# Optimization experiments

Measured on AMD Instinct MI355X. Metric: run time of the kernel, lower is better.

The kernel has to match this reference:

```python
import jax, jax.numpy as jnp
import numpy as np

N_NODES = 100000
N_EDGES = 3200000


def gcn_conv(x, row, col, W, n):
    # PyG GCNConv: x @ W, then D^{-1/2}(A+I)D^{-1/2} aggregation (self-loops added).
    h = x @ W  # [N, out]
    loop = jnp.arange(n)
    r = jnp.concatenate([row, loop])
    c = jnp.concatenate([col, loop])
    deg = jax.ops.segment_sum(jnp.ones_like(c, dtype=h.dtype), c, num_segments=n)
    dinv = jnp.where(deg > 0, jax.lax.rsqrt(deg), 0.0)
    norm = dinv[r] * dinv[c]  # [E+N]
    msg = h[r] * norm[:, None]  # gather + scale
    return jax.ops.segment_sum(msg, c, num_segments=n)  # scatter-add


def setup_inputs() -> dict:
    key = jax.random.key(0)
    k1, k2, k3, k4, k5 = jax.random.split(key, 5)
    x = jax.random.normal(k1, (N_NODES, 1), dtype=jnp.float32)
    edge_index = jax.random.randint(k2, (2, N_EDGES), 0, N_NODES, dtype=jnp.int64)
    W1 = jax.random.normal(k3, (1, 16), dtype=jnp.float32) * 0.5
    W2 = jax.random.normal(k4, (16, 16), dtype=jnp.float32) * 0.25
    W3 = jax.random.normal(k5, (16, 11), dtype=jnp.float32) * 0.25
    b = jnp.zeros((11,), dtype=jnp.float32)
    return {"x": x, "edge_index": edge_index, "W1": W1, "W2": W2, "W3": W3, "b": b}


def reference(x, edge_index, W1, W2, W3, b):
    n = x.shape[0]
    row, col = edge_index[0], edge_index[1]
    h = jax.nn.relu(gcn_conv(x, row, col, W1, n))
    h = jax.nn.relu(gcn_conv(h, row, col, W2, n))
    g = jnp.mean(h, axis=0).reshape(-1, 16)  # [1,16] graph readout
    out = (g @ W3).squeeze() + b  # [11]
    return out
```

## Files before the change

### kernel.cpp

```cpp
#include <hip/hip_runtime.h>

static constexpr int N = 100000;
static constexpr int E = 3200000;
static constexpr int BUKSHIFT = 8;
static constexpr int BUKSZ = 1 << BUKSHIFT;
static constexpr int BUKMASK = BUKSZ - 1;
static constexpr int NBUK = (N + BUKSZ - 1) / BUKSZ;
static constexpr int CAP = 12288;
static constexpr int GSTRIDE = 16;
static constexpr int SC_CHUNK = 4096;
static constexpr int SC_T = 512;
static constexpr int SC_BLOCKS = (E + SC_CHUNK - 1) / SC_CHUNK;


__global__ void k_init(int* __restrict__ gofs) {
    int i = blockIdx.x * blockDim.x + threadIdx.x;
    if (i < NBUK) gofs[i * GSTRIDE] = i * CAP;
}

__global__ __launch_bounds__(SC_T) void k_scatter(const int4* __restrict__ rows4,
                                                  const int4* __restrict__ cols4,
                                                  int* __restrict__ gofs,
                                                  int* __restrict__ binned) {
    __shared__ int hist[4 * NBUK];
    __shared__ int gbase[NBUK];

    const int tid = threadIdx.x;
    const int g = tid >> 7;
    for (int i = tid; i < 4 * NBUK; i += SC_T) hist[i] = 0;
    __syncthreads();

    const int nI4 = E / 4;
    const int base4 = blockIdx.x * (SC_CHUNK / 4);
    const int ia = base4 + tid, ib = base4 + SC_T + tid;
    const bool va = ia < nI4, vb = ib < nI4;
    int4 ra, ca, rb, cb;
    if (va) { ra = rows4[ia]; ca = cols4[ia]; }
    if (vb) { rb = rows4[ib]; cb = cols4[ib]; }

    if (va) {
        atomicAdd(&hist[g * NBUK + (ca.x >> BUKSHIFT)], 1);
        atomicAdd(&hist[g * NBUK + (ca.y >> BUKSHIFT)], 1);
        atomicAdd(&hist[g * NBUK + (ca.z >> BUKSHIFT)], 1);
        atomicAdd(&hist[g * NBUK + (ca.w >> BUKSHIFT)], 1);
    }
    if (vb) {
        atomicAdd(&hist[g * NBUK + (cb.x >> BUKSHIFT)], 1);
        atomicAdd(&hist[g * NBUK + (cb.y >> BUKSHIFT)], 1);
        atomicAdd(&hist[g * NBUK + (cb.z >> BUKSHIFT)], 1);
        atomicAdd(&hist[g * NBUK + (cb.w >> BUKSHIFT)], 1);
    }
    __syncthreads();

    if (tid < NBUK) {
        int h0 = hist[0 * NBUK + tid], h1 = hist[1 * NBUK + tid];
        int h2 = hist[2 * NBUK + tid], h3 = hist[3 * NBUK + tid];
        hist[0 * NBUK + tid] = 0;
        hist[1 * NBUK + tid] = h0;
        hist[2 * NBUK + tid] = h0 + h1;
        hist[3 * NBUK + tid] = h0 + h1 + h2;
        int c = h0 + h1 + h2 + h3;
        gbase[tid] = c ? atomicAdd(&gofs[tid * GSTRIDE], c) : 0;
    }
    __syncthreads();

    if (va) {
        int b, off;
        b = ca.x >> BUKSHIFT; off = atomicAdd(&hist[g * NBUK + b], 1); binned[gbase[b] + off] = (ra.x << BUKSHIFT) | (ca.x & BUKMASK);
        b = ca.y >> BUKSHIFT; off = atomicAdd(&hist[g * NBUK + b], 1); binned[gbase[b] + off] = (ra.y << BUKSHIFT) | (ca.y & BUKMASK);
        b = ca.z >> BUKSHIFT; off = atomicAdd(&hist[g * NBUK + b], 1); binned[gbase[b] + off] = (ra.z << BUKSHIFT) | (ca.z & BUKMASK);
        b = ca.w >> BUKSHIFT; off = atomicAdd(&hist[g * NBUK + b], 1); binned[gbase[b] + off] = (ra.w << BUKSHIFT) | (ca.w & BUKMASK);
    }
    if (vb) {
        int b, off;
        b = cb.x >> BUKSHIFT; off = atomicAdd(&hist[g * NBUK + b], 1); binned[gbase[b] + off] = (rb.x << BUKSHIFT) | (cb.x & BUKMASK);
        b = cb.y >> BUKSHIFT; off = atomicAdd(&hist[g * NBUK + b], 1); binned[gbase[b] + off] = (rb.y << BUKSHIFT) | (cb.y & BUKMASK);
        b = cb.z >> BUKSHIFT; off = atomicAdd(&hist[g * NBUK + b], 1); binned[gbase[b] + off] = (rb.z << BUKSHIFT) | (cb.z & BUKMASK);
        b = cb.w >> BUKSHIFT; off = atomicAdd(&hist[g * NBUK + b], 1); binned[gbase[b] + off] = (rb.w << BUKSHIFT) | (cb.w & BUKMASK);
    }
}

__global__ __launch_bounds__(1024) void k_deg(const int* __restrict__ binned,
                                              const int* __restrict__ gofs,
                                              const float* __restrict__ x,
                                              float* __restrict__ dinv,
                                              float* __restrict__ y1) {
    __shared__ int cnt[8][BUKSZ];
    const int tid = threadIdx.x;
    for (int i = tid; i < 8 * BUKSZ; i += 1024) (&cnt[0][0])[i] = 0;
    __syncthreads();
    const int b = blockIdx.x, g = tid >> 7;
    const int s0 = b * CAP;
    const int n = gofs[b * GSTRIDE] - s0;
    const int n4 = n >> 2;
    const int4* b4 = (const int4*)(binned + s0);
    for (int i = tid; i < n4; i += 1024) {
        int4 p = b4[i];
        atomicAdd(&cnt[g][p.x & BUKMASK], 1);
        atomicAdd(&cnt[g][p.y & BUKMASK], 1);
        atomicAdd(&cnt[g][p.z & BUKMASK], 1);
        atomicAdd(&cnt[g][p.w & BUKMASK], 1);
    }
    if (tid < (n & 3)) atomicAdd(&cnt[g][binned[s0 + (n4 << 2) + tid] & BUKMASK], 1);
    __syncthreads();
    if (tid < BUKSZ) {
        int v = (b << BUKSHIFT) + tid;
        if (v < N) {
            int c = 0;
            #pragma unroll
            for (int q = 0; q < 8; ++q) c += cnt[q][tid];
            float d = rsqrtf(1.0f + (float)c);
            dinv[v] = d;
            y1[v] = d * x[v];
        }
    }
}

__global__ __launch_bounds__(1024) void k_acc1(const int* __restrict__ binned,
                                               const int* __restrict__ gofs,
                                               const float* __restrict__ y1,
                                               const float* __restrict__ dinv,
                                               float* __restrict__ m) {
    __shared__ float acc[8][BUKSZ];
    const int tid = threadIdx.x;
    for (int i = tid; i < 8 * BUKSZ; i += 1024) (&acc[0][0])[i] = 0.f;
    __syncthreads();
    const int b = blockIdx.x, g = tid >> 7;
    const int s0 = b * CAP;
    const int n = gofs[b * GSTRIDE] - s0;
    const int n4 = n >> 2;
    const int4* b4 = (const int4*)(binned + s0);
    for (int i = tid; i < n4; i += 1024) {
        int4 p = b4[i];
        atomicAdd(&acc[g][p.x & BUKMASK], y1[p.x >> BUKSHIFT]);
        atomicAdd(&acc[g][p.y & BUKMASK], y1[p.y >> BUKSHIFT]);
        atomicAdd(&acc[g][p.z & BUKMASK], y1[p.z >> BUKSHIFT]);
        atomicAdd(&acc[g][p.w & BUKMASK], y1[p.w >> BUKSHIFT]);
    }
    if (tid < (n & 3)) {
        int p = binned[s0 + (n4 << 2) + tid];
        atomicAdd(&acc[g][p & BUKMASK], y1[p >> BUKSHIFT]);
    }
    __syncthreads();
    if (tid < BUKSZ) {
        int v = (b << BUKSHIFT) + tid;
        if (v < N) {
            float a = 0.f;
            #pragma unroll
            for (int q = 0; q < 8; ++q) a += acc[q][tid];
            float d = dinv[v];
            float s = d * a + d * y1[v];
            m[v] = d * s;
        }
    }
}

__global__ __launch_bounds__(1024) void k_acc2(const int* __restrict__ binned,
                                               const int* __restrict__ gofs,
                                               const float* __restrict__ m,
                                               const float* __restrict__ dinv,
                                               const float* __restrict__ W1,
                                               const float* __restrict__ W2,
                                               float* __restrict__ partials) {
    __shared__ float tp[8][BUKSZ], tn[8][BUKSZ];
    __shared__ float sP[16], sM[16], sAcc[16];
    const int tid = threadIdx.x;
    if (tid < 16) {
        float p = 0.f, q = 0.f;
        for (int k = 0; k < 16; ++k) {
            float w1 = W1[k];
            float w2 = W2[k * 16 + tid];
            p += fmaxf(w1, 0.f) * w2;
            q += fminf(w1, 0.f) * w2;
        }
        sP[tid] = p; sM[tid] = q; sAcc[tid] = 0.f;
    }
    for (int i = tid; i < 8 * BUKSZ; i += 1024) { (&tp[0][0])[i] = 0.f; (&tn[0][0])[i] = 0.f; }
    __syncthreads();
    const int b = blockIdx.x, g = tid >> 7;
    const int s0 = b * CAP;
    const int n = gofs[b * GSTRIDE] - s0;
    const int n4 = n >> 2;
    const int4* b4 = (const int4*)(binned + s0);
    for (int i = tid; i < n4; i += 1024) {
        int4 p = b4[i];
        float v0 = m[p.x >> BUKSHIFT], v1 = m[p.y >> BUKSHIFT];
        float v2 = m[p.z >> BUKSHIFT], v3 = m[p.w >> BUKSHIFT];
        atomicAdd(v0 >= 0.f ? &tp[g][p.x & BUKMASK] : &tn[g][p.x & BUKMASK], v0);
        atomicAdd(v1 >= 0.f ? &tp[g][p.y & BUKMASK] : &tn[g][p.y & BUKMASK], v1);
        atomicAdd(v2 >= 0.f ? &tp[g][p.z & BUKMASK] : &tn[g][p.z & BUKMASK], v2);
        atomicAdd(v3 >= 0.f ? &tp[g][p.w & BUKMASK] : &tn[g][p.w & BUKMASK], v3);
    }
    if (tid < (n & 3)) {
        int p = binned[s0 + (n4 << 2) + tid];
        float val = m[p >> BUKSHIFT];
        atomicAdd(val >= 0.f ? &tp[g][p & BUKMASK] : &tn[g][p & BUKMASK], val);
    }
    __syncthreads();
    float alpha = 0.f, beta = 0.f;
    if (tid < BUKSZ) {
        int v = (b << BUKSHIFT) + tid;
        if (v < N) {
            float a = 0.f, bb = 0.f;
            #pragma unroll
            for (int q = 0; q < 8; ++q) { a += tp[q][tid]; bb += tn[q][tid]; }
            float d = dinv[v], mv = m[v];
            alpha = d * a;
            beta  = d * bb;
            float self = d * mv;
            if (mv >= 0.f) alpha += self; else beta += self;
        }
    }
    const int lane = tid & 63;
    for (int j = 0; j < 16; ++j) {
        float h = fmaxf(alpha * sP[j] + beta * sM[j], 0.f);
        #pragma unroll
        for (int off = 32; off > 0; off >>= 1) h += __shfl_down(h, off);
        if (lane == 0 && h != 0.f) atomicAdd(&sAcc[j], h);
    }
    __syncthreads();
    if (tid < 16) partials[b * 16 + tid] = sAcc[tid];
}

__global__ void k_out(const float* __restrict__ partials, const float* __restrict__ W3,
                      const float* __restrict__ b, float* __restrict__ out) {
    __shared__ float s[16][16];
    int j = threadIdx.x & 15;
    int g = threadIdx.x >> 4;
    float acc = 0.f;
    for (int blk = g; blk < NBUK; blk += 16) acc += partials[blk * 16 + j];
    s[g][j] = acc;
    __syncthreads();
    if (threadIdx.x < 16) {
        float tot = 0.f;
        #pragma unroll
        for (int gg = 0; gg < 16; ++gg) tot += s[gg][threadIdx.x];
        s[0][threadIdx.x] = tot * (1.0f / (float)N);
    }
    __syncthreads();
    if (threadIdx.x < 11) {
        float acc2 = b[threadIdx.x];
        #pragma unroll
        for (int k = 0; k < 16; ++k) acc2 += s[0][k] * W3[k * 11 + threadIdx.x];
        out[threadIdx.x] = acc2;
    }
}

extern "C" void kernel_launch(void* const* d_in, const int* in_sizes, int n_in,
                              void* d_out, int out_size, void* d_ws, size_t ws_size,
                              hipStream_t stream) {
    const float* x  = (const float*)d_in[0];
    const int*   ei = (const int*)d_in[1];
    const float* W1 = (const float*)d_in[2];
    const float* W2 = (const float*)d_in[3];
    const float* W3 = (const float*)d_in[4];
    const float* b  = (const float*)d_in[5];
    float* out = (float*)d_out;

    int*   wsi      = (int*)d_ws;
    int*   binned   = wsi;
    float* dinv     = (float*)(wsi + (size_t)NBUK * CAP);
    float* y1       = dinv + N;
    float* m        = y1 + N;
    int*   gofs     = (int*)(m + N);
    float* partials = (float*)(gofs + NBUK * GSTRIDE);

    const int4* rows4 = (const int4*)ei;
    const int4* cols4 = (const int4*)(ei + E);

    k_init   <<<1, 512, 0, stream>>>(gofs);
    k_scatter<<<SC_BLOCKS, SC_T, 0, stream>>>(rows4, cols4, gofs, binned);
    k_deg    <<<NBUK, 1024, 0, stream>>>(binned, gofs, x, dinv, y1);
    k_acc1   <<<NBUK, 1024, 0, stream>>>(binned, gofs, y1, dinv, m);
    k_acc2   <<<NBUK, 1024, 0, stream>>>(binned, gofs, m, dinv, W1, W2, partials);
    k_out    <<<1, 256, 0, stream>>>(partials, W3, b, out);
}
```

Before: 118.0 us.

## Split per-bucket aggregation across multiple blocks with global atomic combine

Each bucket's edge list is now processed by four 512-thread blocks instead of one 1024-thread block. Partial sums are combined into global per-node arrays with atomics, and separate elementwise finalize kernels compute dinv, m and the readout. The scatter kernel chunk is halved so more blocks run. The aim is more parallelism, since there are only about 391 buckets for a GPU with many CUs. The cost is extra kernel launches, global atomics, and zero-initialisation of four N-length arrays.

After: 120.4 us. About the same (+2.0%).

```diff
diff --git a/kernel.cpp b/kernel.cpp
--- a/kernel.cpp
+++ b/kernel.cpp
@@ -8,13 +8,18 @@
 static constexpr int NBUK = (N + BUKSZ - 1) / BUKSZ;
 static constexpr int CAP = 12288;
 static constexpr int GSTRIDE = 16;
-static constexpr int SC_CHUNK = 4096;
+static constexpr int SC_CHUNK = 2048;
 static constexpr int SC_T = 512;
 static constexpr int SC_BLOCKS = (E + SC_CHUNK - 1) / SC_CHUNK;
-
-
-__global__ void k_init(int* __restrict__ gofs) {
+static constexpr int S = 4;
+static constexpr int NP2 = (N + 1023) / 1024;
+
+
+__global__ void k_init(int* __restrict__ gofs, int* __restrict__ degg,
+                       float* __restrict__ accg, float* __restrict__ tpg,
+                       float* __restrict__ tng) {
     int i = blockIdx.x * blockDim.x + threadIdx.x;
+    if (i < N) { degg[i] = 0; accg[i] = 0.f; tpg[i] = 0.f; tng[i] = 0.f; }
     if (i < NBUK) gofs[i * GSTRIDE] = i * CAP;
 }
 
@@ -31,24 +36,16 @@
     __syncthreads();
 
     const int nI4 = E / 4;
-    const int base4 = blockIdx.x * (SC_CHUNK / 4);
-    const int ia = base4 + tid, ib = base4 + SC_T + tid;
-    const bool va = ia < nI4, vb = ib < nI4;
-    int4 ra, ca, rb, cb;
+    const int ia = blockIdx.x * (SC_CHUNK / 4) + tid;
+    const bool va = ia < nI4;
+    int4 ra, ca;
     if (va) { ra = rows4[ia]; ca = cols4[ia]; }
-    if (vb) { rb = rows4[ib]; cb = cols4[ib]; }
 
     if (va) {
         atomicAdd(&hist[g * NBUK + (ca.x >> BUKSHIFT)], 1);
         atomicAdd(&hist[g * NBUK + (ca.y >> BUKSHIFT)], 1);
         atomicAdd(&hist[g * NBUK + (ca.z >> BUKSHIFT)], 1);
         atomicAdd(&hist[g * NBUK + (ca.w >> BUKSHIFT)], 1);
-    }
-    if (vb) {
-        atomicAdd(&hist[g * NBUK + (cb.x >> BUKSHIFT)], 1);
-        atomicAdd(&hist[g * NBUK + (cb.y >> BUKSHIFT)], 1);
-        atomicAdd(&hist[g * NBUK + (cb.z >> BUKSHIFT)], 1);
-        atomicAdd(&hist[g * NBUK + (cb.w >> BUKSHIFT)], 1);
     }
     __syncthreads();
 
@@ -71,73 +68,72 @@
         b = ca.z >> BUKSHIFT; off = atomicAdd(&hist[g * NBUK + b], 1); binned[gbase[b] + off] = (ra.z << BUKSHIFT) | (ca.z & BUKMASK);
         b = ca.w >> BUKSHIFT; off = atomicAdd(&hist[g * NBUK + b], 1); binned[gbase[b] + off] = (ra.w << BUKSHIFT) | (ca.w & BUKMASK);
     }
-    if (vb) {
-        int b, off;
-        b = cb.x >> BUKSHIFT; off = atomicAdd(&hist[g * NBUK + b], 1); binned[gbase[b] + off] = (rb.x << BUKSHIFT) | (cb.x & BUKMASK);
-        b = cb.y >> BUKSHIFT; off = atomicAdd(&hist[g * NBUK + b], 1); binned[gbase[b] + off] = (rb.y << BUKSHIFT) | (cb.y & BUKMASK);
-        b = cb.z >> BUKSHIFT; off = atomicAdd(&hist[g * NBUK + b], 1); binned[gbase[b] + off] = (rb.z << BUKSHIFT) | (cb.z & BUKMASK);
-        b = cb.w >> BUKSHIFT; off = atomicAdd(&hist[g * NBUK + b], 1); binned[gbase[b] + off] = (rb.w << BUKSHIFT) | (cb.w & BUKMASK);
-    }
-}
-
-__global__ __launch_bounds__(1024) void k_deg(const int* __restrict__ binned,
-                                              const int* __restrict__ gofs,
-                                              const float* __restrict__ x,
-                                              float* __restrict__ dinv,
-                                              float* __restrict__ y1) {
-    __shared__ int cnt[8][BUKSZ];
-    const int tid = threadIdx.x;
-    for (int i = tid; i < 8 * BUKSZ; i += 1024) (&cnt[0][0])[i] = 0;
-    __syncthreads();
-    const int b = blockIdx.x, g = tid >> 7;
+}
+
+
+__global__ __launch_bounds__(SC_T) void k_degA(const int* __restrict__ binned,
+                                               const int* __restrict__ gofs,
+                                               int* __restrict__ degg) {
+    __shared__ int cnt[4][BUKSZ];
+    const int tid = threadIdx.x;
+    for (int i = tid; i < 4 * BUKSZ; i += SC_T) (&cnt[0][0])[i] = 0;
+    __syncthreads();
+    const int b = blockIdx.x >> 2, s = blockIdx.x & 3, g = tid >> 7;
     const int s0 = b * CAP;
     const int n = gofs[b * GSTRIDE] - s0;
     const int n4 = n >> 2;
+    const int q0 = (n4 * s) / S, q1 = (n4 * (s + 1)) / S;
     const int4* b4 = (const int4*)(binned + s0);
-    for (int i = tid; i < n4; i += 1024) {
+    for (int i = q0 + tid; i < q1; i += SC_T) {
         int4 p = b4[i];
         atomicAdd(&cnt[g][p.x & BUKMASK], 1);
         atomicAdd(&cnt[g][p.y & BUKMASK], 1);
         atomicAdd(&cnt[g][p.z & BUKMASK], 1);
         atomicAdd(&cnt[g][p.w & BUKMASK], 1);
     }
-    if (tid < (n & 3)) atomicAdd(&cnt[g][binned[s0 + (n4 << 2) + tid] & BUKMASK], 1);
+    if (s == S - 1 && tid < (n & 3)) atomicAdd(&cnt[g][binned[s0 + (n4 << 2) + tid] & BUKMASK], 1);
     __syncthreads();
     if (tid < BUKSZ) {
         int v = (b << BUKSHIFT) + tid;
         if (v < N) {
-            int c = 0;
-            #pragma unroll
-            for (int q = 0; q < 8; ++q) c += cnt[q][tid];
-            float d = rsqrtf(1.0f + (float)c);
-            dinv[v] = d;
-            y1[v] = d * x[v];
+            int c = cnt[0][tid] + cnt[1][tid] + cnt[2][tid] + cnt[3][tid];
+            if (c) atomicAdd(&degg[v], c);
         }
     }
 }
 
-__global__ __launch_bounds__(1024) void k_acc1(const int* __restrict__ binned,
-                                               const int* __restrict__ gofs,
-                                               const float* __restrict__ y1,
-                                               const float* __restrict__ dinv,
-                                               float* __restrict__ m) {
-    __shared__ float acc[8][BUKSZ];
-    const int tid = threadIdx.x;
-    for (int i = tid; i < 8 * BUKSZ; i += 1024) (&acc[0][0])[i] = 0.f;
-    __syncthreads();
-    const int b = blockIdx.x, g = tid >> 7;
+__global__ void k_degF(const int* __restrict__ degg, const float* __restrict__ x,
+                       float* __restrict__ dinv, float* __restrict__ y1) {
+    int v = blockIdx.x * blockDim.x + threadIdx.x;
+    if (v < N) {
+        float d = rsqrtf(1.0f + (float)degg[v]);
+        dinv[v] = d;
+        y1[v] = d * x[v];
+    }
+}
+
+__global__ __launch_bounds__(SC_T) void k_acc1A(const int* __restrict__ binned,
+                                                const int* __restrict__ gofs,
+                                                const float* __restrict__ y1,
+                                                float* __restrict__ accg) {
+    __shared__ float acc[4][BUKSZ];
+    const int tid = threadIdx.x;
+    for (int i = tid; i < 4 * BUKSZ; i += SC_T) (&acc[0][0])[i] = 0.f;
+    __syncthreads();
+    const int b = blockIdx.x >> 2, s = blockIdx.x & 3, g = tid >> 7;
     const int s0 = b * CAP;
     const int n = gofs[b * GSTRIDE] - s0;
     const int n4 = n >> 2;
+    const int q0 = (n4 * s) / S, q1 = (n4 * (s + 1)) / S;
     const int4* b4 = (const int4*)(binned + s0);
-    for (int i = tid; i < n4; i += 1024) {
+    for (int i = q0 + tid; i < q1; i += SC_T) {
         int4 p = b4[i];
         atomicAdd(&acc[g][p.x & BUKMASK], y1[p.x >> BUKSHIFT]);
         atomicAdd(&acc[g][p.y & BUKMASK], y1[p.y >> BUKSHIFT]);
         atomicAdd(&acc[g][p.z & BUKMASK], y1[p.z >> BUKSHIFT]);
         atomicAdd(&acc[g][p.w & BUKMASK], y1[p.w >> BUKSHIFT]);
     }
-    if (tid < (n & 3)) {
+    if (s == S - 1 && tid < (n & 3)) {
         int p = binned[s0 + (n4 << 2) + tid];
         atomicAdd(&acc[g][p & BUKMASK], y1[p >> BUKSHIFT]);
     }
@@ -145,24 +141,70 @@
     if (tid < BUKSZ) {
         int v = (b << BUKSHIFT) + tid;
         if (v < N) {
-            float a = 0.f;
-            #pragma unroll
-            for (int q = 0; q < 8; ++q) a += acc[q][tid];
-            float d = dinv[v];
-            float s = d * a + d * y1[v];
-            m[v] = d * s;
+            float a = acc[0][tid] + acc[1][tid] + acc[2][tid] + acc[3][tid];
+            if (a != 0.f) atomicAdd(&accg[v], a);
         }
     }
 }
 
-__global__ __launch_bounds__(1024) void k_acc2(const int* __restrict__ binned,
-                                               const int* __restrict__ gofs,
-                                               const float* __restrict__ m,
-                                               const float* __restrict__ dinv,
-                                               const float* __restrict__ W1,
-                                               const float* __restrict__ W2,
-                                               float* __restrict__ partials) {
-    __shared__ float tp[8][BUKSZ], tn[8][BUKSZ];
+__global__ void k_acc1F(const float* __restrict__ accg, const float* __restrict__ dinv,
+                        const float* __restrict__ y1, float* __restrict__ m) {
+    int v = blockIdx.x * blockDim.x + threadIdx.x;
+    if (v < N) {
+        float d = dinv[v];
+        float s = d * accg[v] + d * y1[v];
+        m[v] = d * s;
+    }
+}
+
+__global__ __launch_bounds__(SC_T) void k_acc2A(const int* __restrict__ binned,
+                                                const int* __restrict__ gofs,
+                                                const float* __restrict__ m,
+                                                float* __restrict__ tpg,
+                                                float* __restrict__ tng) {
+    __shared__ float tp[4][BUKSZ], tn[4][BUKSZ];
+    const int tid = threadIdx.x;
+    for (int i = tid; i < 4 * BUKSZ; i += SC_T) { (&tp[0][0])[i] = 0.f; (&tn[0][0])[i] = 0.f; }
+    __syncthreads();
+    const int b = blockIdx.x >> 2, s = blockIdx.x & 3, g = tid >> 7;
+    const int s0 = b * CAP;
+    const int n = gofs[b * GSTRIDE] - s0;
+    const int n4 = n >> 2;
+    const int q0 = (n4 * s) / S, q1 = (n4 * (s + 1)) / S;
+    const int4* b4 = (const int4*)(binned + s0);
+    for (int i = q0 + tid; i < q1; i += SC_T) {
+        int4 p = b4[i];
+        float v0 = m[p.x >> BUKSHIFT], v1 = m[p.y >> BUKSHIFT];
+        float v2 = m[p.z >> BUKSHIFT], v3 = m[p.w >> BUKSHIFT];
+        atomicAdd(v0 >= 0.f ? &tp[g][p.x & BUKMASK] : &tn[g][p.x & BUKMASK], v0);
+        atomicAdd(v1 >= 0.f ? &tp[g][p.y & BUKMASK] : &tn[g][p.y & BUKMASK], v1);
+        atomicAdd(v2 >= 0.f ? &tp[g][p.z & BUKMASK] : &tn[g][p.z & BUKMASK], v2);
+        atomicAdd(v3 >= 0.f ? &tp[g][p.w & BUKMASK] : &tn[g][p.w & BUKMASK], v3);
+    }
+    if (s == S - 1 && tid < (n & 3)) {
+        int p = binned[s0 + (n4 << 2) + tid];
+        float val = m[p >> BUKSHIFT];
+        atomicAdd(val >= 0.f ? &tp[g][p & BUKMASK] : &tn[g][p & BUKMASK], val);
+    }
+    __syncthreads();
+    if (tid < BUKSZ) {
+        int v = (b << BUKSHIFT) + tid;
+        if (v < N) {
+            float a = tp[0][tid] + tp[1][tid] + tp[2][tid] + tp[3][tid];
+            float c = tn[0][tid] + tn[1][tid] + tn[2][tid] + tn[3][tid];
+            if (a != 0.f) atomicAdd(&tpg[v], a);
+            if (c != 0.f) atomicAdd(&tng[v], c);
+        }
+    }
+}
+
+__global__ __launch_bounds__(1024) void k_acc2F(const float* __restrict__ tpg,
+                                                const float* __restrict__ tng,
+                                                const float* __restrict__ m,
+                                                const float* __restrict__ dinv,
+                                                const float* __restrict__ W1,
+                                                const float* __restrict__ W2,
+                                                float* __restrict__ partials) {
     __shared__ float sP[16], sM[16], sAcc[16];
     const int tid = threadIdx.x;
     if (tid < 16) {
@@ -175,41 +217,15 @@
         }
         sP[tid] = p; sM[tid] = q; sAcc[tid] = 0.f;
     }
-    for (int i = tid; i < 8 * BUKSZ; i += 1024) { (&tp[0][0])[i] = 0.f; (&tn[0][0])[i] = 0.f; }
-    __syncthreads();
-    const int b = blockIdx.x, g = tid >> 7;
-    const int s0 = b * CAP;
-    const int n = gofs[b * GSTRIDE] - s0;
-    const int n4 = n >> 2;
-    const int4* b4 = (const int4*)(binned + s0);
-    for (int i = tid; i < n4; i += 1024) {
-        int4 p = b4[i];
-        float v0 = m[p.x >> BUKSHIFT], v1 = m[p.y >> BUKSHIFT];
-        float v2 = m[p.z >> BUKSHIFT], v3 = m[p.w >> BUKSHIFT];
-        atomicAdd(v0 >= 0.f ? &tp[g][p.x & BUKMASK] : &tn[g][p.x & BUKMASK], v0);
-        atomicAdd(v1 >= 0.f ? &tp[g][p.y & BUKMASK] : &tn[g][p.y & BUKMASK], v1);
-        atomicAdd(v2 >= 0.f ? &tp[g][p.z & BUKMASK] : &tn[g][p.z & BUKMASK], v2);
-        atomicAdd(v3 >= 0.f ? &tp[g][p.w & BUKMASK] : &tn[g][p.w & BUKMASK], v3);
-    }
-    if (tid < (n & 3)) {
-        int p = binned[s0 + (n4 << 2) + tid];
-        float val = m[p >> BUKSHIFT];
-        atomicAdd(val >= 0.f ? &tp[g][p & BUKMASK] : &tn[g][p & BUKMASK], val);
-    }
-    __syncthreads();
+    __syncthreads();
+    const int v = blockIdx.x * 1024 + tid;
     float alpha = 0.f, beta = 0.f;
-    if (tid < BUKSZ) {
-        int v = (b << BUKSHIFT) + tid;
-        if (v < N) {
-            float a = 0.f, bb = 0.f;
-            #pragma unroll
-            for (int q = 0; q < 8; ++q) { a += tp[q][tid]; bb += tn[q][tid]; }
-            float d = dinv[v], mv = m[v];
-            alpha = d * a;
-            beta  = d * bb;
-            float self = d * mv;
-            if (mv >= 0.f) alpha += self; else beta += self;
-        }
+    if (v < N) {
+        float d = dinv[v], mv = m[v];
+        alpha = d * tpg[v];
+        beta  = d * tng[v];
+        float self = d * mv;
+        if (mv >= 0.f) alpha += self; else beta += self;
     }
     const int lane = tid & 63;
     for (int j = 0; j < 16; ++j) {
@@ -219,7 +235,7 @@
         if (lane == 0 && h != 0.f) atomicAdd(&sAcc[j], h);
     }
     __syncthreads();
-    if (tid < 16) partials[b * 16 + tid] = sAcc[tid];
+    if (tid < 16) partials[blockIdx.x * 16 + tid] = sAcc[tid];
 }
 
 __global__ void k_out(const float* __restrict__ partials, const float* __restrict__ W3,
@@ -228,7 +244,7 @@
     int j = threadIdx.x & 15;
     int g = threadIdx.x >> 4;
     float acc = 0.f;
-    for (int blk = g; blk < NBUK; blk += 16) acc += partials[blk * 16 + j];
+    for (int blk = g; blk < NP2; blk += 16) acc += partials[blk * 16 + j];
     s[g][j] = acc;
     __syncthreads();
     if (threadIdx.x < 16) {
@@ -259,19 +275,26 @@
 
     int*   wsi      = (int*)d_ws;
     int*   binned   = wsi;
-    float* dinv     = (float*)(wsi + (size_t)NBUK * CAP);
+    int*   gofs     = wsi + (size_t)NBUK * CAP;
+    int*   degg     = gofs + NBUK * GSTRIDE;
+    float* accg     = (float*)(degg + N);
+    float* tpg      = accg + N;
+    float* tng      = tpg + N;
+    float* dinv     = tng + N;
     float* y1       = dinv + N;
     float* m        = y1 + N;
-    int*   gofs     = (int*)(m + N);
-    float* partials = (float*)(gofs + NBUK * GSTRIDE);
+    float* partials = m + N;
 
     const int4* rows4 = (const int4*)ei;
     const int4* cols4 = (const int4*)(ei + E);
 
-    k_init   <<<1, 512, 0, stream>>>(gofs);
+    k_init   <<<(N + 511) / 512, 512, 0, stream>>>(gofs, degg, accg, tpg, tng);
     k_scatter<<<SC_BLOCKS, SC_T, 0, stream>>>(rows4, cols4, gofs, binned);
-    k_deg    <<<NBUK, 1024, 0, stream>>>(binned, gofs, x, dinv, y1);
-    k_acc1   <<<NBUK, 1024, 0, stream>>>(binned, gofs, y1, dinv, m);
-    k_acc2   <<<NBUK, 1024, 0, stream>>>(binned, gofs, m, dinv, W1, W2, partials);
+    k_degA   <<<NBUK * S, SC_T, 0, stream>>>(binned, gofs, degg);
+    k_degF   <<<(N + 511) / 512, 512, 0, stream>>>(degg, x, dinv, y1);
+    k_acc1A  <<<NBUK * S, SC_T, 0, stream>>>(binned, gofs, y1, accg);
+    k_acc1F  <<<(N + 511) / 512, 512, 0, stream>>>(accg, dinv, y1, m);
+    k_acc2A  <<<NBUK * S, SC_T, 0, stream>>>(binned, gofs, m, tpg, tng);
+    k_acc2F  <<<NP2, 1024, 0, stream>>>(tpg, tng, m, dinv, W1, W2, partials);
     k_out    <<<1, 256, 0, stream>>>(partials, W3, b, out);
 }
```
